# Optimization experiments

Hardware: AMD Instinct MI355X
Metric: run time of the kernel (lower is better)

The kernel has to match this reference:

```python
import jax, jax.numpy as jnp
import numpy as np

B, CIN, COUT, H, W = 16, 64, 64, 128, 128
KH, KW = 3, 3
PAD, STRIDE = 1, 1


def setup_inputs() -> dict:
    key = jax.random.key(0)
    k1, k2 = jax.random.split(key)
    x = jax.random.normal(k1, (B, CIN, H, W), dtype=jnp.float32)
    scale = (1.0 / (CIN * KH * KW)) ** 0.5
    weight = jax.random.normal(k2, (COUT, CIN, KH, KW), dtype=jnp.float32) * scale
    bias = jnp.zeros((COUT,), dtype=jnp.float32)
    return {"x": x, "weight": weight, "bias": bias}


def reference(x, weight, bias):
    # Faithful translation of FFTConv2d.forward (including its einsum semantics:
    # 'bchw,oihw->bohw' sums over c and i independently, as in the torch source).
    b, c, h, w = x.shape
    kh, kw = weight.shape[2], weight.shape[3]
    pad_h = h + kh - 1  # 130
    pad_w = w + kw - 1  # 130
    x_padded = jnp.pad(x, ((0, 0), (0, 0), (0, pad_h - h), (0, pad_w - w)))
    w_padded = jnp.pad(weight, ((0, 0), (0, 0), (0, pad_h - kh), (0, pad_w - kw)))
    X_fft = jnp.fft.rfft2(x_padded)                  # [B,C,pad_h,pad_w//2+1]
    W_fft = jnp.fft.rfft2(w_padded, s=(pad_h, pad_w))  # [O,I,pad_h,pad_w//2+1]
    Y_fft = jnp.einsum('bchw,oihw->bohw', X_fft, W_fft)
    y = jnp.fft.irfft2(Y_fft, s=(pad_h, pad_w))      # [B,O,pad_h,pad_w]
    # torch: y[:, :, padding:-padding or None:stride, padding:-padding or None:stride]
    y = y[:, :, PAD:-PAD:STRIDE, PAD:-PAD:STRIDE]    # [B,O,H,W] for PAD=1,STRIDE=1
    y = y + bias[None, :, None, None]
    return y
```

## Files before the change

kernel.cpp:

```cpp
#include <hip/hip_runtime.h>

typedef float f32x4 __attribute__((ext_vector_type(4)));

#define NB 16
#define NC 64
#define NH 128
#define NW 128
#define STRIPE 8
#define LROWS (STRIPE + 2)
#define LCOLS 136

__global__ __launch_bounds__(256) void fused_conv_kernel(
    const float* __restrict__ x, const float* __restrict__ wgt,
    const float* __restrict__ bias, float* __restrict__ out) {
  __shared__ float xs[LROWS][LCOLS];
  __shared__ float red[64][9][4];
  __shared__ float wl[64][12];

  const int t   = threadIdx.x;
  const int bid = blockIdx.x;
  const int b   = bid >> 4;
  const int R0  = (bid & 15) * STRIPE;

  {
    const int lr = t >> 5;
    const int g  = t & 31;
    const int ir = R0 - 1 + lr;
    f32x4 a0 = {0,0,0,0}, a1 = {0,0,0,0}, a2 = {0,0,0,0}, a3 = {0,0,0,0};
    if (ir >= 0 && ir < NH) {
      const float* xp = x + (b * NC * NH + ir) * NW + g * 4;
      #pragma unroll 4
      for (int c = 0; c < NC; c += 4) {
        a0 += *(const f32x4*)(xp + (c + 0) * (NH * NW));
        a1 += *(const f32x4*)(xp + (c + 1) * (NH * NW));
        a2 += *(const f32x4*)(xp + (c + 2) * (NH * NW));
        a3 += *(const f32x4*)(xp + (c + 3) * (NH * NW));
      }
    }
    *(f32x4*)&xs[lr][4 + g * 4] = (a0 + a1) + (a2 + a3);

    if (t < 64) {
      const int lr2 = 8 + (t >> 5);
      const int ir2 = R0 - 1 + lr2;
      f32x4 c0 = {0,0,0,0}, c1 = {0,0,0,0}, c2 = {0,0,0,0}, c3 = {0,0,0,0};
      if (ir2 >= 0 && ir2 < NH) {
        const float* xp = x + (b * NC * NH + ir2) * NW + g * 4;
        #pragma unroll 4
        for (int c = 0; c < NC; c += 4) {
          c0 += *(const f32x4*)(xp + (c + 0) * (NH * NW));
          c1 += *(const f32x4*)(xp + (c + 1) * (NH * NW));
          c2 += *(const f32x4*)(xp + (c + 2) * (NH * NW));
          c3 += *(const f32x4*)(xp + (c + 3) * (NH * NW));
        }
      }
      *(f32x4*)&xs[lr2][4 + g * 4] = (c0 + c1) + (c2 + c3);
    }
    if (t < 2 * LROWS) xs[t >> 1][(t & 1) ? 132 : 3] = 0.f;
  }

  {
    const int o  = t >> 2;
    const int qr = t & 3;
    const float* wp = wgt + o * (NC * 9) + qr * (16 * 9);
    float part[9] = {0.f, 0.f, 0.f, 0.f, 0.f, 0.f, 0.f, 0.f, 0.f};
    #pragma unroll
    for (int i = 0; i < 16; ++i) {
      #pragma unroll
      for (int k = 0; k < 9; ++k) part[k] += wp[i * 9 + k];
    }
    #pragma unroll
    for (int k = 0; k < 9; ++k) red[o][k][qr] = part[k];
  }
  __syncthreads();

  for (int s2 = t; s2 < 576; s2 += 256) {
    int o  = s2 / 9;
    int t9 = s2 - o * 9;
    wl[o][8 - t9] = red[o][t9][0] + red[o][t9][1] + red[o][t9][2] + red[o][t9][3];
  }
  if (t < 64) wl[t][9] = bias[t];
  __syncthreads();

  {
    const int ro = t >> 5;
    const int g  = t & 31;
    const int q0 = g * 4;
    float X0[6], X1[6], X2[6];
    #pragma unroll
    for (int m = 0; m < 6; ++m) {
      X0[m] = xs[ro][q0 + 3 + m];
      X1[m] = xs[ro + 1][q0 + 3 + m];
      X2[m] = xs[ro + 2][q0 + 3 + m];
    }
    float* op = out + ((b * 64) * NH + R0 + ro) * NW + q0;
    for (int o = 0; o < 64; ++o) {
      f32x4 wa = *(const f32x4*)&wl[o][0];
      f32x4 wb = *(const f32x4*)&wl[o][4];
      f32x4 wc = *(const f32x4*)&wl[o][8];
      f32x4 y;
      #pragma unroll
      for (int jj = 0; jj < 4; ++jj) {
        float acc = wc[1];
        acc += wa[0] * X0[jj] + wa[1] * X0[jj + 1] + wa[2] * X0[jj + 2];
        acc += wa[3] * X1[jj] + wb[0] * X1[jj + 1] + wb[1] * X1[jj + 2];
        acc += wb[2] * X2[jj] + wb[3] * X2[jj + 1] + wc[0] * X2[jj + 2];
        y[jj] = acc;
      }
      *(f32x4*)(op + o * (NH * NW)) = y;
    }
  }
}

extern "C" void kernel_launch(void* const* d_in, const int* in_sizes, int n_in,
                              void* d_out, int out_size, void* d_ws, size_t ws_size,
                              hipStream_t stream) {
  const float* x    = (const float*)d_in[0];
  const float* wgt  = (const float*)d_in[1];
  const float* bias = (const float*)d_in[2];
  float* out = (float*)d_out;
  (void)in_sizes; (void)n_in; (void)out_size; (void)d_ws; (void)ws_size;

  fused_conv_kernel<<<dim3(NB * (NH / STRIPE)), dim3(256), 0, stream>>>(x, wgt, bias, out);
}
```

Baseline: 120.1 us.

## Double block size to split halo loads, weight reduction and output channels

Raises the block to 512 threads. 320 threads each load one of the 10 halo rows of the channel-summed input, and the remaining 192 threads sum the weights over channel thirds in parallel, instead of 64 threads doing a second serial pass. In the output phase each half of the block produces 32 of the 64 output channels, which halves the per-thread store loop. This adds more threads per block and can lower how many blocks fit per CU, but it removes the serialized tail in the load phase.

```diff
diff --git a/kernel.cpp b/kernel.cpp
--- a/kernel.cpp
+++ b/kernel.cpp
@@ -10,11 +10,11 @@
 #define LROWS (STRIPE + 2)
 #define LCOLS 136
 
-__global__ __launch_bounds__(256) void fused_conv_kernel(
+__global__ __launch_bounds__(512) void fused_conv_kernel(
     const float* __restrict__ x, const float* __restrict__ wgt,
     const float* __restrict__ bias, float* __restrict__ out) {
   __shared__ float xs[LROWS][LCOLS];
-  __shared__ float red[64][9][4];
+  __shared__ float red[64][9][3];
   __shared__ float wl[64][12];
 
   const int t   = threadIdx.x;
@@ -22,10 +22,10 @@
   const int b   = bid >> 4;
   const int R0  = (bid & 15) * STRIPE;
 
-  {
-    const int lr = t >> 5;
-    const int g  = t & 31;
-    const int ir = R0 - 1 + lr;
+  if (t < 320) {
+    const int row = t >> 5;
+    const int g   = t & 31;
+    const int ir  = R0 - 1 + row;
     f32x4 a0 = {0,0,0,0}, a1 = {0,0,0,0}, a2 = {0,0,0,0}, a3 = {0,0,0,0};
     if (ir >= 0 && ir < NH) {
       const float* xp = x + (b * NC * NH + ir) * NW + g * 4;
@@ -37,54 +37,39 @@
         a3 += *(const f32x4*)(xp + (c + 3) * (NH * NW));
       }
     }
-    *(f32x4*)&xs[lr][4 + g * 4] = (a0 + a1) + (a2 + a3);
-
-    if (t < 64) {
-      const int lr2 = 8 + (t >> 5);
-      const int ir2 = R0 - 1 + lr2;
-      f32x4 c0 = {0,0,0,0}, c1 = {0,0,0,0}, c2 = {0,0,0,0}, c3 = {0,0,0,0};
-      if (ir2 >= 0 && ir2 < NH) {
-        const float* xp = x + (b * NC * NH + ir2) * NW + g * 4;
-        #pragma unroll 4
-        for (int c = 0; c < NC; c += 4) {
-          c0 += *(const f32x4*)(xp + (c + 0) * (NH * NW));
-          c1 += *(const f32x4*)(xp + (c + 1) * (NH * NW));
-          c2 += *(const f32x4*)(xp + (c + 2) * (NH * NW));
-          c3 += *(const f32x4*)(xp + (c + 3) * (NH * NW));
-        }
-      }
-      *(f32x4*)&xs[lr2][4 + g * 4] = (c0 + c1) + (c2 + c3);
-    }
+    *(f32x4*)&xs[row][4 + g * 4] = (a0 + a1) + (a2 + a3);
     if (t < 2 * LROWS) xs[t >> 1][(t & 1) ? 132 : 3] = 0.f;
-  }
-
-  {
-    const int o  = t >> 2;
-    const int qr = t & 3;
-    const float* wp = wgt + o * (NC * 9) + qr * (16 * 9);
+  } else {
+    const int idx   = t - 320;
+    const int o     = idx / 3;
+    const int third = idx - o * 3;
+    const int c0    = (third * NC) / 3;
+    const int c1    = ((third + 1) * NC) / 3;
+    const float* wp = wgt + o * (NC * 9);
     float part[9] = {0.f, 0.f, 0.f, 0.f, 0.f, 0.f, 0.f, 0.f, 0.f};
-    #pragma unroll
-    for (int i = 0; i < 16; ++i) {
+    for (int i = c0; i < c1; ++i) {
       #pragma unroll
       for (int k = 0; k < 9; ++k) part[k] += wp[i * 9 + k];
     }
     #pragma unroll
-    for (int k = 0; k < 9; ++k) red[o][k][qr] = part[k];
+    for (int k = 0; k < 9; ++k) red[o][k][third] = part[k];
   }
   __syncthreads();
 
-  for (int s2 = t; s2 < 576; s2 += 256) {
-    int o  = s2 / 9;
-    int t9 = s2 - o * 9;
-    wl[o][8 - t9] = red[o][t9][0] + red[o][t9][1] + red[o][t9][2] + red[o][t9][3];
+  for (int s = t; s < 576; s += 512) {
+    int o  = s / 9;
+    int t9 = s - o * 9;
+    wl[o][8 - t9] = red[o][t9][0] + red[o][t9][1] + red[o][t9][2];
   }
   if (t < 64) wl[t][9] = bias[t];
   __syncthreads();
 
   {
-    const int ro = t >> 5;
-    const int g  = t & 31;
-    const int q0 = g * 4;
+    const int ohalf = t >> 8;
+    const int r5    = t & 255;
+    const int ro    = r5 >> 5;
+    const int g     = r5 & 31;
+    const int q0    = g * 4;
     float X0[6], X1[6], X2[6];
     #pragma unroll
     for (int m = 0; m < 6; ++m) {
@@ -92,8 +77,9 @@
       X1[m] = xs[ro + 1][q0 + 3 + m];
       X2[m] = xs[ro + 2][q0 + 3 + m];
     }
-    float* op = out + ((b * 64) * NH + R0 + ro) * NW + q0;
-    for (int o = 0; o < 64; ++o) {
+    float* op = out + ((b * 64 + ohalf * 32) * NH + R0 + ro) * NW + q0;
+    for (int oi = 0; oi < 32; ++oi) {
+      const int o = ohalf * 32 + oi;
       f32x4 wa = *(const f32x4*)&wl[o][0];
       f32x4 wb = *(const f32x4*)&wl[o][4];
       f32x4 wc = *(const f32x4*)&wl[o][8];
@@ -106,7 +92,7 @@
         acc += wb[2] * X2[jj] + wb[3] * X2[jj + 1] + wc[0] * X2[jj + 2];
         y[jj] = acc;
       }
-      *(f32x4*)(op + o * (NH * NW)) = y;
+      *(f32x4*)(op + oi * (NH * NW)) = y;
     }
   }
 }
@@ -120,5 +106,5 @@
   float* out = (float*)d_out;
   (void)in_sizes; (void)n_in; (void)out_size; (void)d_ws; (void)ws_size;
 
-  fused_conv_kernel<<<dim3(NB * (NH / STRIPE)), dim3(256), 0, stream>>>(x, wgt, bias, out);
+  fused_conv_kernel<<<dim3(NB * (NH / STRIPE)), dim3(512), 0, stream>>>(x, wgt, bias, out);
 }
```

Measured after the change: 123.7 us. 1.03x slower.
